# Optimization experiments

Hardware: AMD Instinct MI355X
Metric: run time of the kernel (lower is better)

The kernel has to match this reference:

```python
import jax, jax.numpy as jnp
import numpy as np

B, T, C, H = 8, 2048, 768, 64  # batch, block_size, n_embd, head_size

def setup_inputs() -> dict:
    key = jax.random.key(0)
    kx, kk, kq, kv = jax.random.split(key, 4)
    x = jax.random.normal(kx, (B, T, C), dtype=jnp.float32)
    Wk = jax.random.normal(kk, (C, H), dtype=jnp.float32) * (C ** -0.5)
    Wq = jax.random.normal(kq, (C, H), dtype=jnp.float32) * (C ** -0.5)
    Wv = jax.random.normal(kv, (C, H), dtype=jnp.float32) * (C ** -0.5)
    return {"x": x, "Wk": Wk, "Wq": Wq, "Wv": Wv}

def reference(x, Wk, Wq, Wv):
    # single causal self-attention head (dropout in eval mode = identity)
    k = jnp.einsum('btc,ch->bth', x, Wk)  # [B,T,H]
    q = jnp.einsum('btc,ch->bth', x, Wq)
    v = jnp.einsum('btc,ch->bth', x, Wv)
    scale = jnp.asarray(k.shape[-1], x.dtype) ** -0.5
    wei = jnp.einsum('bth,bsh->bts', q, k) * scale  # [B,T,T]
    t = x.shape[1]
    causal = jnp.tril(jnp.ones((t, t), dtype=bool))
    wei = jnp.where(causal[None, :, :], wei, jnp.asarray(-jnp.inf, wei.dtype))
    wei = jax.nn.softmax(wei, axis=-1)
    out = jnp.einsum('bts,bsh->bth', wei, v)  # [B,T,H]
    return out
```

## Files before the change

### kernel.cpp

```cpp
#include <hip/hip_runtime.h>
#include <hip/hip_bf16.h>

typedef __attribute__((ext_vector_type(8))) short short8;
typedef __attribute__((ext_vector_type(4))) float f32x4;

#define B_  8
#define T_  2048
#define C_  768
#define H_  64
#define M_  (B_ * T_)

static __device__ __forceinline__ unsigned short f2bf(float f) {
    __hip_bfloat16 h = __float2bfloat16(f);
    return *reinterpret_cast<unsigned short*>(&h);
}

static __device__ __forceinline__ short8 make_frag(const unsigned short* p0, const unsigned short* p1) {
    const ushort4 a = *reinterpret_cast<const ushort4*>(p0);
    const ushort4 b = *reinterpret_cast<const ushort4*>(p1);
    short8 r;
    r[0] = (short)a.x; r[1] = (short)a.y; r[2] = (short)a.z; r[3] = (short)a.w;
    r[4] = (short)b.x; r[5] = (short)b.y; r[6] = (short)b.z; r[7] = (short)b.w;
    return r;
}

static __device__ __forceinline__ int swz(int row, int u) {
    return row * 64 + ((((u) >> 3) ^ (row & 7)) << 3) + (u & 7);
}

__global__ __launch_bounds__(256) void prep_w(
    const float* __restrict__ Wq, const float* __restrict__ Wk, const float* __restrict__ Wv,
    unsigned short* __restrict__ Wt) {

    const int t   = threadIdx.x;
    const int mat = blockIdx.x / 48;
    const int kb  = blockIdx.x % 48;
    const int h   = t & 63;
    const int k0  = (kb * 4 + (t >> 6)) * 4;

    const float* Ws = (mat == 0) ? Wq : (mat == 1) ? Wk : Wv;
    ushort4 o;
    o.x = f2bf(Ws[(size_t)(k0 + 0) * H_ + h]);
    o.y = f2bf(Ws[(size_t)(k0 + 1) * H_ + h]);
    o.z = f2bf(Ws[(size_t)(k0 + 2) * H_ + h]);
    o.w = f2bf(Ws[(size_t)(k0 + 3) * H_ + h]);
    *reinterpret_cast<ushort4*>(&Wt[(size_t)(mat * 64 + h) * C_ + k0]) = o;
}

__global__ __launch_bounds__(256) void proj_kernel(
    const float* __restrict__ x, const unsigned short* __restrict__ Wt,
    unsigned short* __restrict__ qkv) {

    __shared__ unsigned short Als[4 * 12 * 512];

    const int tid = threadIdx.x;
    const int w   = tid >> 6;
    const int l   = tid & 63;
    const int lg  = l >> 4;
    const int lc  = l & 15;
    const int row0 = blockIdx.x * 64;

    const int sr  = tid >> 2;
    const int so  = tid & 3;
    const int srt = sr >> 4;
    const int sr15 = sr & 15;
    const int sbase = (so * 16 + (sr15 ^ so)) * 8;

    f32x4 acc[4][3];
#pragma unroll
    for (int rt = 0; rt < 4; ++rt)
#pragma unroll
        for (int ct = 0; ct < 3; ++ct) acc[rt][ct] = (f32x4)0.f;

    const unsigned short* bbase[3];
#pragma unroll
    for (int ct = 0; ct < 3; ++ct)
        bbase[ct] = Wt + (size_t)(w * 48 + ct * 16 + lc) * C_ + lg * 8;

    for (int phase = 0; phase < 2; ++phase) {
        if (phase) __syncthreads();
#pragma unroll
        for (int g = 0; g < 3; ++g) {
            float4 fa[4][2];
#pragma unroll
            for (int jj = 0; jj < 4; ++jj) {
                const int j = g * 4 + jj;
                const float* xp = x + (size_t)(row0 + sr) * C_ + phase * 384 + j * 32 + so * 8;
                fa[jj][0] = *reinterpret_cast<const float4*>(xp);
                fa[jj][1] = *reinterpret_cast<const float4*>(xp + 4);
            }
#pragma unroll
            for (int jj = 0; jj < 4; ++jj) {
                const int j = g * 4 + jj;
                short8 v;
                v[0] = (short)f2bf(fa[jj][0].x); v[1] = (short)f2bf(fa[jj][0].y);
                v[2] = (short)f2bf(fa[jj][0].z); v[3] = (short)f2bf(fa[jj][0].w);
                v[4] = (short)f2bf(fa[jj][1].x); v[5] = (short)f2bf(fa[jj][1].y);
                v[6] = (short)f2bf(fa[jj][1].z); v[7] = (short)f2bf(fa[jj][1].w);
                *reinterpret_cast<short8*>(&Als[(srt * 12 + j) * 512 + sbase]) = v;
            }
        }
        __syncthreads();

        short8 bcur[3], bnxt[3];
#pragma unroll
        for (int ct = 0; ct < 3; ++ct)
            bcur[ct] = *reinterpret_cast<const short8*>(bbase[ct] + phase * 384);

#pragma unroll
        for (int kk = 0; kk < 12; ++kk) {
            if (kk < 11) {
#pragma unroll
                for (int ct = 0; ct < 3; ++ct)
                    bnxt[ct] = *reinterpret_cast<const short8*>(bbase[ct] + phase * 384 + (kk + 1) * 32);
            }
            short8 af[4];
#pragma unroll
            for (int rt = 0; rt < 4; ++rt)
                af[rt] = *reinterpret_cast<const short8*>(
                    &Als[(rt * 12 + kk) * 512 + (lg * 16 + (lc ^ lg)) * 8]);
#pragma unroll
            for (int rt = 0; rt < 4; ++rt)
#pragma unroll
                for (int ct = 0; ct < 3; ++ct)
                    acc[rt][ct] = __builtin_amdgcn_mfma_f32_16x16x32_bf16(af[rt], bcur[ct], acc[rt][ct], 0, 0, 0);
            if (kk < 11) {
#pragma unroll
                for (int ct = 0; ct < 3; ++ct) bcur[ct] = bnxt[ct];
            }
        }
    }

#pragma unroll
    for (int ct = 0; ct < 3; ++ct) {
        const int col = w * 48 + ct * 16 + lc;
        const int mat = col >> 6;
        const int h   = col & 63;
#pragma unroll
        for (int rt = 0; rt < 4; ++rt)
#pragma unroll
            for (int j = 0; j < 4; ++j) {
                const int grow = row0 + rt * 16 + lg * 4 + j;
                qkv[(size_t)mat * (M_ * H_) + (size_t)grow * H_ + h] = f2bf(acc[rt][ct][j]);
            }
    }
}

#define SEG_FLOATS 4224
#define LOG2E_SCALE 0.18033688011112042f

template<int SEG>
static __device__ __forceinline__ int segs_per_batch() { return SEG == 32 ? 32 : 80; }

template<int SEG>
static __device__ __forceinline__ void decode_seg(int r, int& qt, int& seg) {
    if (SEG == 32) { qt = r; seg = 0; return; }
    if (r < 8)       { qt = r;                seg = 0; }
    else if (r < 24) { qt = 8  + (r - 8) / 2; seg = (r - 8) & 1; }
    else if (r < 48) { qt = 16 + (r - 24) / 3; seg = (r - 24) % 3; }
    else             { qt = 24 + (r - 48) / 4; seg = (r - 48) & 3; }
}

template<int SEG>
static __device__ __forceinline__ int seg_prefix(int qt) {
    if (SEG == 32) return qt;
    if (qt < 8)  return qt;
    if (qt < 16) return 8  + 2 * (qt - 8);
    if (qt < 24) return 24 + 3 * (qt - 16);
    return 48 + 4 * (qt - 24);
}

template<int SEG>
__global__ __launch_bounds__(256) void attn_partial(
    const unsigned short* __restrict__ qkv, float* __restrict__ part) {

    const int spb = segs_per_batch<SEG>();
    const int b   = blockIdx.x / spb;
    const int r_  = blockIdx.x % spb;
    int qt, seg;
    decode_seg<SEG>(r_, qt, seg);

    const int tid = threadIdx.x;
    const int w  = tid >> 6;
    const int l  = tid & 63;
    const int lg = l >> 4;
    const int lc = l & 15;

    __shared__ unsigned short Kl[64 * 64];
    __shared__ unsigned short Vt[64 * 64];

    const unsigned short* Qg = qkv;
    const unsigned short* Kg = qkv + (size_t)M_ * H_;
    const unsigned short* Vg = qkv + (size_t)2 * M_ * H_;

    const unsigned short* qrow = Qg + (size_t)(b * T_ + qt * 64 + w * 16 + lc) * H_;
    short8 qf[2];
#pragma unroll
    for (int ks = 0; ks < 2; ++ks)
        qf[ks] = make_frag(qrow + ks * 32 + lg * 4, qrow + ks * 32 + lg * 4 + 16);

    float mval = -1e30f, lsum = 0.f;
    f32x4 oT[4];
#pragma unroll
    for (int t = 0; t < 4; ++t) oT[t] = (f32x4)0.f;

    const int q_glob = qt * 64 + w * 16 + lc;

    const int kv_beg = seg * SEG;
    const int kv_end = min(kv_beg + SEG, qt + 1);

    for (int kv = kv_beg; kv < kv_end; ++kv) {
        __syncthreads();
#pragma unroll
        for (int rep = 0; rep < 2; ++rep) {
            const int idx = rep * 256 + tid;
            const int s   = idx >> 3;
            const int c16 = idx & 7;
            const size_t g = (size_t)(b * T_ + kv * 64 + s) * H_ + c16 * 8;
            short8 kvec = *reinterpret_cast<const short8*>(&Kg[g]);
            *reinterpret_cast<short8*>(&Kl[s * 64 + ((c16 ^ (s & 7)) << 3)]) = kvec;
        }
#pragma unroll
        for (int rep = 0; rep < 2; ++rep) {
            const int idx = rep * 256 + tid;
            const int s2  = idx >> 4;
            const int h0  = (idx & 15) * 4;
            const int s   = 2 * s2;
            const size_t g = (size_t)(b * T_ + kv * 64 + s) * H_ + h0;
            ushort4 v0 = *reinterpret_cast<const ushort4*>(&Vg[g]);
            ushort4 v1 = *reinterpret_cast<const ushort4*>(&Vg[g + H_]);
#pragma unroll
            for (int j = 0; j < 4; ++j) {
                const int h = h0 + j;
                unsigned int pk = (unsigned int)(&v0.x)[j] | ((unsigned int)(&v1.x)[j] << 16);
                *reinterpret_cast<unsigned int*>(&Vt[swz(h, s)]) = pk;
            }
        }
        __syncthreads();

        f32x4 sT[4];
#pragma unroll
        for (int st = 0; st < 4; ++st) {
            f32x4 accs = (f32x4)0.f;
#pragma unroll
            for (int ks = 0; ks < 2; ++ks) {
                const short8 kf = make_frag(&Kl[swz(st * 16 + lc, ks * 32 + lg * 4)],
                                            &Kl[swz(st * 16 + lc, ks * 32 + lg * 4 + 16)]);
                accs = __builtin_amdgcn_mfma_f32_16x16x32_bf16(kf, qf[ks], accs, 0, 0, 0);
            }
            sT[st] = accs;
        }

        float p[4][4];
#pragma unroll
        for (int st = 0; st < 4; ++st)
#pragma unroll
            for (int r = 0; r < 4; ++r)
                p[st][r] = sT[st][r] * LOG2E_SCALE;

        if (kv == qt) {
#pragma unroll
            for (int st = 0; st < 4; ++st)
#pragma unroll
                for (int r = 0; r < 4; ++r)
                    if ((kv * 64 + st * 16 + lg * 4 + r) > q_glob) p[st][r] = -1e30f;
        }

        float pm[4];
#pragma unroll
        for (int st = 0; st < 4; ++st)
            pm[st] = fmaxf(fmaxf(p[st][0], p[st][1]), fmaxf(p[st][2], p[st][3]));
        float pmax = fmaxf(fmaxf(pm[0], pm[1]), fmaxf(pm[2], pm[3]));
        pmax = fmaxf(pmax, __shfl_xor(pmax, 16));
        pmax = fmaxf(pmax, __shfl_xor(pmax, 32));

        const float mnew  = fmaxf(mval, pmax);
        const float alpha = exp2f(mval - mnew);
        mval = mnew;

        float ps[4];
#pragma unroll
        for (int st = 0; st < 4; ++st) {
#pragma unroll
            for (int r = 0; r < 4; ++r)
                p[st][r] = exp2f(p[st][r] - mnew);
            ps[st] = (p[st][0] + p[st][1]) + (p[st][2] + p[st][3]);
        }
        float srow = (ps[0] + ps[1]) + (ps[2] + ps[3]);
        srow += __shfl_xor(srow, 16);
        srow += __shfl_xor(srow, 32);
        lsum = lsum * alpha + srow;

#pragma unroll
        for (int ht = 0; ht < 4; ++ht) oT[ht] *= alpha;

        short8 pb[2];
#pragma unroll
        for (int ks = 0; ks < 2; ++ks) {
#pragma unroll
            for (int r = 0; r < 4; ++r) {
                pb[ks][r]     = (short)f2bf(p[2 * ks][r]);
                pb[ks][r + 4] = (short)f2bf(p[2 * ks + 1][r]);
            }
        }

#pragma unroll
        for (int ks = 0; ks < 2; ++ks) {
#pragma unroll
            for (int ht = 0; ht < 4; ++ht) {
                const short8 vf = make_frag(&Vt[swz(ht * 16 + lc, ks * 32 + lg * 4)],
                                            &Vt[swz(ht * 16 + lc, ks * 32 + lg * 4 + 16)]);
                oT[ht] = __builtin_amdgcn_mfma_f32_16x16x32_bf16(vf, pb[ks], oT[ht], 0, 0, 0);
            }
        }
    }

    float* base = part + (size_t)blockIdx.x * SEG_FLOATS;
#pragma unroll
    for (int ht = 0; ht < 4; ++ht)
        *reinterpret_cast<f32x4*>(&base[(w * 16 + lc) * 64 + ht * 16 + lg * 4]) = oT[ht];
    if (lg == 0) {
        base[4096 + w * 16 + lc] = mval;
        base[4160 + w * 16 + lc] = lsum;
    }
}

template<int SEG>
__global__ __launch_bounds__(256) void attn_merge(
    const float* __restrict__ part, float* __restrict__ out) {

    const int b  = blockIdx.x >> 5;
    const int qt = blockIdx.x & 31;
    const int nseg = (SEG == 32) ? 1 : (qt / 8 + 1);
    const int spb  = segs_per_batch<SEG>();
    const float* base0 = part + (size_t)(b * spb + seg_prefix<SEG>(qt)) * SEG_FLOATS;

    const int tid = threadIdx.x;
    const int row = tid >> 2;
    const int c0  = (tid & 3) * 16;

    float M = -1e30f;
    for (int s = 0; s < nseg; ++s)
        M = fmaxf(M, base0[(size_t)s * SEG_FLOATS + 4096 + row]);

    float L = 0.f;
    f32x4 acc[4];
#pragma unroll
    for (int k = 0; k < 4; ++k) acc[k] = (f32x4)0.f;

    for (int s = 0; s < nseg; ++s) {
        const float* sb = base0 + (size_t)s * SEG_FLOATS;
        const float wsc = exp2f(sb[4096 + row] - M);
        L += sb[4160 + row] * wsc;
#pragma unroll
        for (int k = 0; k < 4; ++k) {
            const f32x4 ov = *reinterpret_cast<const f32x4*>(&sb[row * 64 + c0 + 4 * k]);
            acc[k] += ov * wsc;
        }
    }
    const float inv = 1.f / L;
    float* op = out + (size_t)(b * T_ + qt * 64 + row) * H_ + c0;
#pragma unroll
    for (int k = 0; k < 4; ++k)
        *reinterpret_cast<f32x4*>(&op[4 * k]) = acc[k] * inv;
}

__global__ __launch_bounds__(256) void attn_kernel(
    const unsigned short* __restrict__ qkv, float* __restrict__ out) {

    const int b  = blockIdx.x >> 5;
    const int qt = blockIdx.x & 31;
    const int tid = threadIdx.x;
    const int w  = tid >> 6;
    const int l  = tid & 63;
    const int lg = l >> 4;
    const int lc = l & 15;

    __shared__ unsigned short Kl[64 * 64];
    __shared__ unsigned short Vt[64 * 64];

    const unsigned short* Qg = qkv;
    const unsigned short* Kg = qkv + (size_t)M_ * H_;
    const unsigned short* Vg = qkv + (size_t)2 * M_ * H_;

    const unsigned short* qrow = Qg + (size_t)(b * T_ + qt * 64 + w * 16 + lc) * H_;
    short8 qf[2];
#pragma unroll
    for (int ks = 0; ks < 2; ++ks)
        qf[ks] = make_frag(qrow + ks * 32 + lg * 4, qrow + ks * 32 + lg * 4 + 16);

    float mval = -1e30f, lsum = 0.f;
    f32x4 oT[4];
#pragma unroll
    for (int t = 0; t < 4; ++t) oT[t] = (f32x4)0.f;

    const int q_glob = qt * 64 + w * 16 + lc;

    for (int kv = 0; kv <= qt; ++kv) {
        __syncthreads();
#pragma unroll
        for (int rep = 0; rep < 2; ++rep) {
            const int idx = rep * 256 + tid;
            const int s   = idx >> 3;
            const int c16 = idx & 7;
            const size_t g = (size_t)(b * T_ + kv * 64 + s) * H_ + c16 * 8;
            short8 kvec = *reinterpret_cast<const short8*>(&Kg[g]);
            *reinterpret_cast<short8*>(&Kl[s * 64 + ((c16 ^ (s & 7)) << 3)]) = kvec;
        }
#pragma unroll
        for (int rep = 0; rep < 2; ++rep) {
            const int idx = rep * 256 + tid;
            const int s2  = idx >> 4;
            const int h0  = (idx & 15) * 4;
            const int s   = 2 * s2;
            const size_t g = (size_t)(b * T_ + kv * 64 + s) * H_ + h0;
            ushort4 v0 = *reinterpret_cast<const ushort4*>(&Vg[g]);
            ushort4 v1 = *reinterpret_cast<const ushort4*>(&Vg[g + H_]);
#pragma unroll
            for (int j = 0; j < 4; ++j) {
                const int h = h0 + j;
                unsigned int pk = (unsigned int)(&v0.x)[j] | ((unsigned int)(&v1.x)[j] << 16);
                *reinterpret_cast<unsigned int*>(&Vt[swz(h, s)]) = pk;
            }
        }
        __syncthreads();

        f32x4 sT[4];
#pragma unroll
        for (int st = 0; st < 4; ++st) {
            f32x4 accs = (f32x4)0.f;
#pragma unroll
            for (int ks = 0; ks < 2; ++ks) {
                const short8 kf = make_frag(&Kl[swz(st * 16 + lc, ks * 32 + lg * 4)],
                                            &Kl[swz(st * 16 + lc, ks * 32 + lg * 4 + 16)]);
                accs = __builtin_amdgcn_mfma_f32_16x16x32_bf16(kf, qf[ks], accs, 0, 0, 0);
            }
            sT[st] = accs;
        }

        float p[4][4];
#pragma unroll
        for (int st = 0; st < 4; ++st)
#pragma unroll
            for (int r = 0; r < 4; ++r)
                p[st][r] = sT[st][r] * LOG2E_SCALE;

        if (kv == qt) {
#pragma unroll
            for (int st = 0; st < 4; ++st)
#pragma unroll
                for (int r = 0; r < 4; ++r)
                    if ((kv * 64 + st * 16 + lg * 4 + r) > q_glob) p[st][r] = -1e30f;
        }

        float pm[4];
#pragma unroll
        for (int st = 0; st < 4; ++st)
            pm[st] = fmaxf(fmaxf(p[st][0], p[st][1]), fmaxf(p[st][2], p[st][3]));
        float pmax = fmaxf(fmaxf(pm[0], pm[1]), fmaxf(pm[2], pm[3]));
        pmax = fmaxf(pmax, __shfl_xor(pmax, 16));
        pmax = fmaxf(pmax, __shfl_xor(pmax, 32));

        const float mnew  = fmaxf(mval, pmax);
        const float alpha = exp2f(mval - mnew);
        mval = mnew;

        float ps[4];
#pragma unroll
        for (int st = 0; st < 4; ++st) {
#pragma unroll
            for (int r = 0; r < 4; ++r)
                p[st][r] = exp2f(p[st][r] - mnew);
            ps[st] = (p[st][0] + p[st][1]) + (p[st][2] + p[st][3]);
        }
        float srow = (ps[0] + ps[1]) + (ps[2] + ps[3]);
        srow += __shfl_xor(srow, 16);
        srow += __shfl_xor(srow, 32);
        lsum = lsum * alpha + srow;

#pragma unroll
        for (int ht = 0; ht < 4; ++ht) oT[ht] *= alpha;

        short8 pb[2];
#pragma unroll
        for (int ks = 0; ks < 2; ++ks) {
#pragma unroll
            for (int r = 0; r < 4; ++r) {
                pb[ks][r]     = (short)f2bf(p[2 * ks][r]);
                pb[ks][r + 4] = (short)f2bf(p[2 * ks + 1][r]);
            }
        }

#pragma unroll
        for (int ks = 0; ks < 2; ++ks) {
#pragma unroll
            for (int ht = 0; ht < 4; ++ht) {
                const short8 vf = make_frag(&Vt[swz(ht * 16 + lc, ks * 32 + lg * 4)],
                                            &Vt[swz(ht * 16 + lc, ks * 32 + lg * 4 + 16)]);
                oT[ht] = __builtin_amdgcn_mfma_f32_16x16x32_bf16(vf, pb[ks], oT[ht], 0, 0, 0);
            }
        }
    }

    const float inv = 1.f / lsum;
    float* op = out + (size_t)(b * T_ + q_glob) * H_;
#pragma unroll
    for (int ht = 0; ht < 4; ++ht) {
        f32x4 v = oT[ht] * inv;
        *reinterpret_cast<f32x4*>(&op[ht * 16 + lg * 4]) = v;
    }
}

extern "C" void kernel_launch(void* const* d_in, const int* in_sizes, int n_in,
                              void* d_out, int out_size, void* d_ws, size_t ws_size,
                              hipStream_t stream) {
    const float* x  = (const float*)d_in[0];
    const float* Wk = (const float*)d_in[1];
    const float* Wq = (const float*)d_in[2];
    const float* Wv = (const float*)d_in[3];

    const size_t qkvB = (size_t)3 * M_ * H_ * 2;
    const size_t WtB  = (size_t)3 * H_ * C_ * 2;
    unsigned short* qkv = (unsigned short*)d_ws;
    unsigned short* Wt  = (unsigned short*)((char*)d_ws + qkvB);
    float* part = (float*)((char*)d_ws + qkvB + WtB);
    float* out  = (float*)d_out;

    prep_w<<<dim3(144), dim3(256), 0, stream>>>(Wq, Wk, Wv, Wt);
    proj_kernel<<<dim3(M_ / 64), dim3(256), 0, stream>>>(x, Wt, qkv);

    const size_t need8  = qkvB + WtB + (size_t)(B_ * 80) * SEG_FLOATS * 4;
    const size_t need32 = qkvB + WtB + (size_t)(B_ * 32) * SEG_FLOATS * 4;
    if (ws_size >= need8) {
        attn_partial<8><<<dim3(B_ * 80), dim3(256), 0, stream>>>(qkv, part);
        attn_merge<8><<<dim3(B_ * 32), dim3(256), 0, stream>>>(part, out);
    } else if (ws_size >= need32) {
        attn_partial<32><<<dim3(B_ * 32), dim3(256), 0, stream>>>(qkv, part);
        attn_merge<32><<<dim3(B_ * 32), dim3(256), 0, stream>>>(part, out);
    } else {
        attn_kernel<<<dim3(B_ * 32), dim3(256), 0, stream>>>(qkv, out);
    }
}
```

Baseline: 64.34 us.

## Halve projection row tile, prefetch K/V tiles into registers, skip redundant rescale

The projection kernel now handles 32 rows per block instead of 64, which doubles the grid and halves LDS use and accumulator registers, so more blocks can be resident. The attention partial kernel loads the next K/V tile into registers while computing on the current tile in shared memory, overlapping global loads with MFMA and softmax work. Both attention kernels skip the online-softmax rescale when no row maximum grew, avoiding the exp2 and the multiplies over the output accumulators. The costs are extra registers for the prefetch buffers and a wave-wide vote per iteration.

```diff
diff --git a/kernel.cpp b/kernel.cpp
--- a/kernel.cpp
+++ b/kernel.cpp
@@ -51,24 +51,23 @@
     const float* __restrict__ x, const unsigned short* __restrict__ Wt,
     unsigned short* __restrict__ qkv) {
 
-    __shared__ unsigned short Als[4 * 12 * 512];
+    __shared__ unsigned short Als[2 * 12 * 512];
 
     const int tid = threadIdx.x;
     const int w   = tid >> 6;
     const int l   = tid & 63;
     const int lg  = l >> 4;
     const int lc  = l & 15;
-    const int row0 = blockIdx.x * 64;
-
-    const int sr  = tid >> 2;
-    const int so  = tid & 3;
-    const int srt = sr >> 4;
+    const int row0 = blockIdx.x * 32;
+
+    const int sr   = tid >> 3;
+    const int so   = tid & 7;
+    const int srt  = sr >> 4;
     const int sr15 = sr & 15;
-    const int sbase = (so * 16 + (sr15 ^ so)) * 8;
-
-    f32x4 acc[4][3];
-#pragma unroll
-    for (int rt = 0; rt < 4; ++rt)
+
+    f32x4 acc[2][3];
+#pragma unroll
+    for (int rt = 0; rt < 2; ++rt)
 #pragma unroll
         for (int ct = 0; ct < 3; ++ct) acc[rt][ct] = (f32x4)0.f;
 
@@ -79,26 +78,25 @@
 
     for (int phase = 0; phase < 2; ++phase) {
         if (phase) __syncthreads();
-#pragma unroll
-        for (int g = 0; g < 3; ++g) {
-            float4 fa[4][2];
-#pragma unroll
-            for (int jj = 0; jj < 4; ++jj) {
-                const int j = g * 4 + jj;
-                const float* xp = x + (size_t)(row0 + sr) * C_ + phase * 384 + j * 32 + so * 8;
-                fa[jj][0] = *reinterpret_cast<const float4*>(xp);
-                fa[jj][1] = *reinterpret_cast<const float4*>(xp + 4);
-            }
-#pragma unroll
-            for (int jj = 0; jj < 4; ++jj) {
-                const int j = g * 4 + jj;
-                short8 v;
-                v[0] = (short)f2bf(fa[jj][0].x); v[1] = (short)f2bf(fa[jj][0].y);
-                v[2] = (short)f2bf(fa[jj][0].z); v[3] = (short)f2bf(fa[jj][0].w);
-                v[4] = (short)f2bf(fa[jj][1].x); v[5] = (short)f2bf(fa[jj][1].y);
-                v[6] = (short)f2bf(fa[jj][1].z); v[7] = (short)f2bf(fa[jj][1].w);
-                *reinterpret_cast<short8*>(&Als[(srt * 12 + j) * 512 + sbase]) = v;
-            }
+        float4 fa[6][2];
+#pragma unroll
+        for (int g = 0; g < 6; ++g) {
+            const float* xp = x + (size_t)(row0 + sr) * C_ + phase * 384 + (so + 8 * g) * 8;
+            fa[g][0] = *reinterpret_cast<const float4*>(xp);
+            fa[g][1] = *reinterpret_cast<const float4*>(xp + 4);
+        }
+#pragma unroll
+        for (int g = 0; g < 6; ++g) {
+            const int j8  = so + 8 * g;
+            const int kk  = j8 >> 2;
+            const int so4 = j8 & 3;
+            short8 v;
+            v[0] = (short)f2bf(fa[g][0].x); v[1] = (short)f2bf(fa[g][0].y);
+            v[2] = (short)f2bf(fa[g][0].z); v[3] = (short)f2bf(fa[g][0].w);
+            v[4] = (short)f2bf(fa[g][1].x); v[5] = (short)f2bf(fa[g][1].y);
+            v[6] = (short)f2bf(fa[g][1].z); v[7] = (short)f2bf(fa[g][1].w);
+            *reinterpret_cast<short8*>(
+                &Als[(srt * 12 + kk) * 512 + (so4 * 16 + (sr15 ^ so4)) * 8]) = v;
         }
         __syncthreads();
 
@@ -114,13 +112,13 @@
                 for (int ct = 0; ct < 3; ++ct)
                     bnxt[ct] = *reinterpret_cast<const short8*>(bbase[ct] + phase * 384 + (kk + 1) * 32);
             }
-            short8 af[4];
-#pragma unroll
-            for (int rt = 0; rt < 4; ++rt)
+            short8 af[2];
+#pragma unroll
+            for (int rt = 0; rt < 2; ++rt)
                 af[rt] = *reinterpret_cast<const short8*>(
                     &Als[(rt * 12 + kk) * 512 + (lg * 16 + (lc ^ lg)) * 8]);
 #pragma unroll
-            for (int rt = 0; rt < 4; ++rt)
+            for (int rt = 0; rt < 2; ++rt)
 #pragma unroll
                 for (int ct = 0; ct < 3; ++ct)
                     acc[rt][ct] = __builtin_amdgcn_mfma_f32_16x16x32_bf16(af[rt], bcur[ct], acc[rt][ct], 0, 0, 0);
@@ -137,7 +135,7 @@
         const int mat = col >> 6;
         const int h   = col & 63;
 #pragma unroll
-        for (int rt = 0; rt < 4; ++rt)
+        for (int rt = 0; rt < 2; ++rt)
 #pragma unroll
             for (int j = 0; j < 4; ++j) {
                 const int grow = row0 + rt * 16 + lg * 4 + j;
@@ -193,6 +191,16 @@
     const unsigned short* Kg = qkv + (size_t)M_ * H_;
     const unsigned short* Vg = qkv + (size_t)2 * M_ * H_;
 
+    const int sK0 = tid >> 3;
+    const int c16 = tid & 7;
+    const int kOff  = sK0 * H_ + c16 * 8;
+    const int kLds0 = sK0 * 64 + ((c16 ^ (sK0 & 7)) << 3);
+    const int kLds1 = (sK0 + 32) * 64 + ((c16 ^ ((sK0 + 32) & 7)) << 3);
+
+    const int sV0 = 2 * (tid >> 4);
+    const int h0  = (tid & 15) * 4;
+    const int vOff = sV0 * H_ + h0;
+
     const unsigned short* qrow = Qg + (size_t)(b * T_ + qt * 64 + w * 16 + lc) * H_;
     short8 qf[2];
 #pragma unroll
@@ -209,7 +217,197 @@
     const int kv_beg = seg * SEG;
     const int kv_end = min(kv_beg + SEG, qt + 1);
 
+    short8  kreg0, kreg1;
+    ushort4 va0, vb0, va1, vb1;
+
+    auto load_tiles = [&](int kv) {
+        const size_t off = (size_t)(b * T_ + kv * 64) * H_;
+        kreg0 = *reinterpret_cast<const short8*>(&Kg[off + kOff]);
+        kreg1 = *reinterpret_cast<const short8*>(&Kg[off + kOff + 32 * H_]);
+        va0 = *reinterpret_cast<const ushort4*>(&Vg[off + vOff]);
+        vb0 = *reinterpret_cast<const ushort4*>(&Vg[off + vOff + H_]);
+        va1 = *reinterpret_cast<const ushort4*>(&Vg[off + vOff + 32 * H_]);
+        vb1 = *reinterpret_cast<const ushort4*>(&Vg[off + vOff + 32 * H_ + H_]);
+    };
+
+    load_tiles(kv_beg);
+
     for (int kv = kv_beg; kv < kv_end; ++kv) {
+        __syncthreads();
+        *reinterpret_cast<short8*>(&Kl[kLds0]) = kreg0;
+        *reinterpret_cast<short8*>(&Kl[kLds1]) = kreg1;
+#pragma unroll
+        for (int j = 0; j < 4; ++j) {
+            const unsigned int p0 = (unsigned int)(&va0.x)[j] | ((unsigned int)(&vb0.x)[j] << 16);
+            *reinterpret_cast<unsigned int*>(&Vt[swz(h0 + j, sV0)]) = p0;
+            const unsigned int p1 = (unsigned int)(&va1.x)[j] | ((unsigned int)(&vb1.x)[j] << 16);
+            *reinterpret_cast<unsigned int*>(&Vt[swz(h0 + j, sV0 + 32)]) = p1;
+        }
+        __syncthreads();
+
+        if (kv + 1 < kv_end) load_tiles(kv + 1);
+
+        f32x4 sT[4];
+#pragma unroll
+        for (int st = 0; st < 4; ++st) {
+            f32x4 accs = (f32x4)0.f;
+#pragma unroll
+            for (int ks = 0; ks < 2; ++ks) {
+                const short8 kf = make_frag(&Kl[swz(st * 16 + lc, ks * 32 + lg * 4)],
+                                            &Kl[swz(st * 16 + lc, ks * 32 + lg * 4 + 16)]);
+                accs = __builtin_amdgcn_mfma_f32_16x16x32_bf16(kf, qf[ks], accs, 0, 0, 0);
+            }
+            sT[st] = accs;
+        }
+
+        float p[4][4];
+#pragma unroll
+        for (int st = 0; st < 4; ++st)
+#pragma unroll
+            for (int r = 0; r < 4; ++r)
+                p[st][r] = sT[st][r] * LOG2E_SCALE;
+
+        if (kv == qt) {
+#pragma unroll
+            for (int st = 0; st < 4; ++st)
+#pragma unroll
+                for (int r = 0; r < 4; ++r)
+                    if ((kv * 64 + st * 16 + lg * 4 + r) > q_glob) p[st][r] = -1e30f;
+        }
+
+        float pm[4];
+#pragma unroll
+        for (int st = 0; st < 4; ++st)
+            pm[st] = fmaxf(fmaxf(p[st][0], p[st][1]), fmaxf(p[st][2], p[st][3]));
+        float pmax = fmaxf(fmaxf(pm[0], pm[1]), fmaxf(pm[2], pm[3]));
+        pmax = fmaxf(pmax, __shfl_xor(pmax, 16));
+        pmax = fmaxf(pmax, __shfl_xor(pmax, 32));
+
+        if (!__all(pmax <= mval)) {
+            const float mnew  = fmaxf(mval, pmax);
+            const float alpha = exp2f(mval - mnew);
+            mval = mnew;
+            lsum *= alpha;
+#pragma unroll
+            for (int ht = 0; ht < 4; ++ht) oT[ht] *= alpha;
+        }
+
+        float ps[4];
+#pragma unroll
+        for (int st = 0; st < 4; ++st) {
+#pragma unroll
+            for (int r = 0; r < 4; ++r)
+                p[st][r] = exp2f(p[st][r] - mval);
+            ps[st] = (p[st][0] + p[st][1]) + (p[st][2] + p[st][3]);
+        }
+        float srow = (ps[0] + ps[1]) + (ps[2] + ps[3]);
+        srow += __shfl_xor(srow, 16);
+        srow += __shfl_xor(srow, 32);
+        lsum += srow;
+
+        short8 pb[2];
+#pragma unroll
+        for (int ks = 0; ks < 2; ++ks) {
+#pragma unroll
+            for (int r = 0; r < 4; ++r) {
+                pb[ks][r]     = (short)f2bf(p[2 * ks][r]);
+                pb[ks][r + 4] = (short)f2bf(p[2 * ks + 1][r]);
+            }
+        }
+
+#pragma unroll
+        for (int ks = 0; ks < 2; ++ks) {
+#pragma unroll
+            for (int ht = 0; ht < 4; ++ht) {
+                const short8 vf = make_frag(&Vt[swz(ht * 16 + lc, ks * 32 + lg * 4)],
+                                            &Vt[swz(ht * 16 + lc, ks * 32 + lg * 4 + 16)]);
+                oT[ht] = __builtin_amdgcn_mfma_f32_16x16x32_bf16(vf, pb[ks], oT[ht], 0, 0, 0);
+            }
+        }
+    }
+
+    float* base = part + (size_t)blockIdx.x * SEG_FLOATS;
+#pragma unroll
+    for (int ht = 0; ht < 4; ++ht)
+        *reinterpret_cast<f32x4*>(&base[(w * 16 + lc) * 64 + ht * 16 + lg * 4]) = oT[ht];
+    if (lg == 0) {
+        base[4096 + w * 16 + lc] = mval;
+        base[4160 + w * 16 + lc] = lsum;
+    }
+}
+
+template<int SEG>
+__global__ __launch_bounds__(256) void attn_merge(
+    const float* __restrict__ part, float* __restrict__ out) {
+
+    const int b  = blockIdx.x >> 5;
+    const int qt = blockIdx.x & 31;
+    const int nseg = (SEG == 32) ? 1 : (qt / 8 + 1);
+    const int spb  = segs_per_batch<SEG>();
+    const float* base0 = part + (size_t)(b * spb + seg_prefix<SEG>(qt)) * SEG_FLOATS;
+
+    const int tid = threadIdx.x;
+    const int row = tid >> 2;
+    const int c0  = (tid & 3) * 16;
+
+    float M = -1e30f;
+    for (int s = 0; s < nseg; ++s)
+        M = fmaxf(M, base0[(size_t)s * SEG_FLOATS + 4096 + row]);
+
+    float L = 0.f;
+    f32x4 acc[4];
+#pragma unroll
+    for (int k = 0; k < 4; ++k) acc[k] = (f32x4)0.f;
+
+    for (int s = 0; s < nseg; ++s) {
+        const float* sb = base0 + (size_t)s * SEG_FLOATS;
+        const float wsc = exp2f(sb[4096 + row] - M);
+        L += sb[4160 + row] * wsc;
+#pragma unroll
+        for (int k = 0; k < 4; ++k) {
+            const f32x4 ov = *reinterpret_cast<const f32x4*>(&sb[row * 64 + c0 + 4 * k]);
+            acc[k] += ov * wsc;
+        }
+    }
+    const float inv = 1.f / L;
+    float* op = out + (size_t)(b * T_ + qt * 64 + row) * H_ + c0;
+#pragma unroll
+    for (int k = 0; k < 4; ++k)
+        *reinterpret_cast<f32x4*>(&op[4 * k]) = acc[k] * inv;
+}
+
+__global__ __launch_bounds__(256) void attn_kernel(
+    const unsigned short* __restrict__ qkv, float* __restrict__ out) {
+
+    const int b  = blockIdx.x >> 5;
+    const int qt = blockIdx.x & 31;
+    const int tid = threadIdx.x;
+    const int w  = tid >> 6;
+    const int l  = tid & 63;
+    const int lg = l >> 4;
+    const int lc = l & 15;
+
+    __shared__ unsigned short Kl[64 * 64];
+    __shared__ unsigned short Vt[64 * 64];
+
+    const unsigned short* Qg = qkv;
+    const unsigned short* Kg = qkv + (size_t)M_ * H_;
+    const unsigned short* Vg = qkv + (size_t)2 * M_ * H_;
+
+    const unsigned short* qrow = Qg + (size_t)(b * T_ + qt * 64 + w * 16 + lc) * H_;
+    short8 qf[2];
+#pragma unroll
+    for (int ks = 0; ks < 2; ++ks)
+        qf[ks] = make_frag(qrow + ks * 32 + lg * 4, qrow + ks * 32 + lg * 4 + 16);
+
+    float mval = -1e30f, lsum = 0.f;
+    f32x4 oT[4];
+#pragma unroll
+    for (int t = 0; t < 4; ++t) oT[t] = (f32x4)0.f;
+
+    const int q_glob = qt * 64 + w * 16 + lc;
+
+    for (int kv = 0; kv <= qt; ++kv) {
         __syncthreads();
 #pragma unroll
         for (int rep = 0; rep < 2; ++rep) {
@@ -274,212 +472,27 @@
         pmax = fmaxf(pmax, __shfl_xor(pmax, 16));
         pmax = fmaxf(pmax, __shfl_xor(pmax, 32));
 
-        const float mnew  = fmaxf(mval, pmax);
-        const float alpha = exp2f(mval - mnew);
-        mval = mnew;
+        if (!__all(pmax <= mval)) {
+            const float mnew  = fmaxf(mval, pmax);
+            const float alpha = exp2f(mval - mnew);
+            mval = mnew;
+            lsum *= alpha;
+#pragma unroll
+            for (int ht = 0; ht < 4; ++ht) oT[ht] *= alpha;
+        }
 
         float ps[4];
 #pragma unroll
         for (int st = 0; st < 4; ++st) {
 #pragma unroll
             for (int r = 0; r < 4; ++r)
-                p[st][r] = exp2f(p[st][r] - mnew);
+                p[st][r] = exp2f(p[st][r] - mval);
             ps[st] = (p[st][0] + p[st][1]) + (p[st][2] + p[st][3]);
         }
         float srow = (ps[0] + ps[1]) + (ps[2] + ps[3]);
         srow += __shfl_xor(srow, 16);
         srow += __shfl_xor(srow, 32);
-        lsum = lsum * alpha + srow;
-
-#pragma unroll
-        for (int ht = 0; ht < 4; ++ht) oT[ht] *= alpha;
-
-        short8 pb[2];
-#pragma unroll
-        for (int ks = 0; ks < 2; ++ks) {
-#pragma unroll
-            for (int r = 0; r < 4; ++r) {
-                pb[ks][r]     = (short)f2bf(p[2 * ks][r]);
-                pb[ks][r + 4] = (short)f2bf(p[2 * ks + 1][r]);
-            }
-        }
-
-#pragma unroll
-        for (int ks = 0; ks < 2; ++ks) {
-#pragma unroll
-            for (int ht = 0; ht < 4; ++ht) {
-                const short8 vf = make_frag(&Vt[swz(ht * 16 + lc, ks * 32 + lg * 4)],
-                                            &Vt[swz(ht * 16 + lc, ks * 32 + lg * 4 + 16)]);
-                oT[ht] = __builtin_amdgcn_mfma_f32_16x16x32_bf16(vf, pb[ks], oT[ht], 0, 0, 0);
-            }
-        }
-    }
-
-    float* base = part + (size_t)blockIdx.x * SEG_FLOATS;
-#pragma unroll
-    for (int ht = 0; ht < 4; ++ht)
-        *reinterpret_cast<f32x4*>(&base[(w * 16 + lc) * 64 + ht * 16 + lg * 4]) = oT[ht];
-    if (lg == 0) {
-        base[4096 + w * 16 + lc] = mval;
-        base[4160 + w * 16 + lc] = lsum;
-    }
-}
-
-template<int SEG>
-__global__ __launch_bounds__(256) void attn_merge(
-    const float* __restrict__ part, float* __restrict__ out) {
-
-    const int b  = blockIdx.x >> 5;
-    const int qt = blockIdx.x & 31;
-    const int nseg = (SEG == 32) ? 1 : (qt / 8 + 1);
-    const int spb  = segs_per_batch<SEG>();
-    const float* base0 = part + (size_t)(b * spb + seg_prefix<SEG>(qt)) * SEG_FLOATS;
-
-    const int tid = threadIdx.x;
-    const int row = tid >> 2;
-    const int c0  = (tid & 3) * 16;
-
-    float M = -1e30f;
-    for (int s = 0; s < nseg; ++s)
-        M = fmaxf(M, base0[(size_t)s * SEG_FLOATS + 4096 + row]);
-
-    float L = 0.f;
-    f32x4 acc[4];
-#pragma unroll
-    for (int k = 0; k < 4; ++k) acc[k] = (f32x4)0.f;
-
-    for (int s = 0; s < nseg; ++s) {
-        const float* sb = base0 + (size_t)s * SEG_FLOATS;
-        const float wsc = exp2f(sb[4096 + row] - M);
-        L += sb[4160 + row] * wsc;
-#pragma unroll
-        for (int k = 0; k < 4; ++k) {
-            const f32x4 ov = *reinterpret_cast<const f32x4*>(&sb[row * 64 + c0 + 4 * k]);
-            acc[k] += ov * wsc;
-        }
-    }
-    const float inv = 1.f / L;
-    float* op = out + (size_t)(b * T_ + qt * 64 + row) * H_ + c0;
-#pragma unroll
-    for (int k = 0; k < 4; ++k)
-        *reinterpret_cast<f32x4*>(&op[4 * k]) = acc[k] * inv;
-}
-
-__global__ __launch_bounds__(256) void attn_kernel(
-    const unsigned short* __restrict__ qkv, float* __restrict__ out) {
-
-    const int b  = blockIdx.x >> 5;
-    const int qt = blockIdx.x & 31;
-    const int tid = threadIdx.x;
-    const int w  = tid >> 6;
-    const int l  = tid & 63;
-    const int lg = l >> 4;
-    const int lc = l & 15;
-
-    __shared__ unsigned short Kl[64 * 64];
-    __shared__ unsigned short Vt[64 * 64];
-
-    const unsigned short* Qg = qkv;
-    const unsigned short* Kg = qkv + (size_t)M_ * H_;
-    const unsigned short* Vg = qkv + (size_t)2 * M_ * H_;
-
-    const unsigned short* qrow = Qg + (size_t)(b * T_ + qt * 64 + w * 16 + lc) * H_;
-    short8 qf[2];
-#pragma unroll
-    for (int ks = 0; ks < 2; ++ks)
-        qf[ks] = make_frag(qrow + ks * 32 + lg * 4, qrow + ks * 32 + lg * 4 + 16);
-
-    float mval = -1e30f, lsum = 0.f;
-    f32x4 oT[4];
-#pragma unroll
-    for (int t = 0; t < 4; ++t) oT[t] = (f32x4)0.f;
-
-    const int q_glob = qt * 64 + w * 16 + lc;
-
-    for (int kv = 0; kv <= qt; ++kv) {
-        __syncthreads();
-#pragma unroll
-        for (int rep = 0; rep < 2; ++rep) {
-            const int idx = rep * 256 + tid;
-            const int s   = idx >> 3;
-            const int c16 = idx & 7;
-            const size_t g = (size_t)(b * T_ + kv * 64 + s) * H_ + c16 * 8;
-            short8 kvec = *reinterpret_cast<const short8*>(&Kg[g]);
-            *reinterpret_cast<short8*>(&Kl[s * 64 + ((c16 ^ (s & 7)) << 3)]) = kvec;
-        }
-#pragma unroll
-        for (int rep = 0; rep < 2; ++rep) {
-            const int idx = rep * 256 + tid;
-            const int s2  = idx >> 4;
-            const int h0  = (idx & 15) * 4;
-            const int s   = 2 * s2;
-            const size_t g = (size_t)(b * T_ + kv * 64 + s) * H_ + h0;
-            ushort4 v0 = *reinterpret_cast<const ushort4*>(&Vg[g]);
-            ushort4 v1 = *reinterpret_cast<const ushort4*>(&Vg[g + H_]);
-#pragma unroll
-            for (int j = 0; j < 4; ++j) {
-                const int h = h0 + j;
-                unsigned int pk = (unsigned int)(&v0.x)[j] | ((unsigned int)(&v1.x)[j] << 16);
-                *reinterpret_cast<unsigned int*>(&Vt[swz(h, s)]) = pk;
-            }
-        }
-        __syncthreads();
-
-        f32x4 sT[4];
-#pragma unroll
-        for (int st = 0; st < 4; ++st) {
-            f32x4 accs = (f32x4)0.f;
-#pragma unroll
-            for (int ks = 0; ks < 2; ++ks) {
-                const short8 kf = make_frag(&Kl[swz(st * 16 + lc, ks * 32 + lg * 4)],
-                                            &Kl[swz(st * 16 + lc, ks * 32 + lg * 4 + 16)]);
-                accs = __builtin_amdgcn_mfma_f32_16x16x32_bf16(kf, qf[ks], accs, 0, 0, 0);
-            }
-            sT[st] = accs;
-        }
-
-        float p[4][4];
-#pragma unroll
-        for (int st = 0; st < 4; ++st)
-#pragma unroll
-            for (int r = 0; r < 4; ++r)
-                p[st][r] = sT[st][r] * LOG2E_SCALE;
-
-        if (kv == qt) {
-#pragma unroll
-            for (int st = 0; st < 4; ++st)
-#pragma unroll
-                for (int r = 0; r < 4; ++r)
-                    if ((kv * 64 + st * 16 + lg * 4 + r) > q_glob) p[st][r] = -1e30f;
-        }
-
-        float pm[4];
-#pragma unroll
-        for (int st = 0; st < 4; ++st)
-            pm[st] = fmaxf(fmaxf(p[st][0], p[st][1]), fmaxf(p[st][2], p[st][3]));
-        float pmax = fmaxf(fmaxf(pm[0], pm[1]), fmaxf(pm[2], pm[3]));
-        pmax = fmaxf(pmax, __shfl_xor(pmax, 16));
-        pmax = fmaxf(pmax, __shfl_xor(pmax, 32));
-
-        const float mnew  = fmaxf(mval, pmax);
-        const float alpha = exp2f(mval - mnew);
-        mval = mnew;
-
-        float ps[4];
-#pragma unroll
-        for (int st = 0; st < 4; ++st) {
-#pragma unroll
-            for (int r = 0; r < 4; ++r)
-                p[st][r] = exp2f(p[st][r] - mnew);
-            ps[st] = (p[st][0] + p[st][1]) + (p[st][2] + p[st][3]);
-        }
-        float srow = (ps[0] + ps[1]) + (ps[2] + ps[3]);
-        srow += __shfl_xor(srow, 16);
-        srow += __shfl_xor(srow, 32);
-        lsum = lsum * alpha + srow;
-
-#pragma unroll
-        for (int ht = 0; ht < 4; ++ht) oT[ht] *= alpha;
+        lsum += srow;
 
         short8 pb[2];
 #pragma unroll
@@ -527,7 +540,7 @@
     float* out  = (float*)d_out;
 
     prep_w<<<dim3(144), dim3(256), 0, stream>>>(Wq, Wk, Wv, Wt);
-    proj_kernel<<<dim3(M_ / 64), dim3(256), 0, stream>>>(x, Wt, qkv);
+    proj_kernel<<<dim3(M_ / 32), dim3(256), 0, stream>>>(x, Wt, qkv);
 
     const size_t need8  = qkvB + WtB + (size_t)(B_ * 80) * SEG_FLOATS * 4;
     const size_t need32 = qkvB + WtB + (size_t)(B_ * 32) * SEG_FLOATS * 4;
```

After: 66.84 us. 3.9% more time.

## Pre-swizzle K/V tiles in projection and double-buffer attention loads via global_load_lds

Applied to the files above, without the earlier changes.

The projection kernel now writes K and V in per-64-row tile images that already carry the swizzled LDS layout, with V stored transposed. The attention kernels can then copy tiles straight into shared memory. The partial-attention kernel double-buffers K/V with direct global-to-LDS loads, prefetching the next tile while computing the current one, and manual waitcnt and barriers replace the transpose-and-store staging. Both attention kernels also skip the online-softmax rescale when no row max grows. This adds scattered, uncoalesced stores in the projection epilogue and depends on hand-written vmcnt accounting being correct.

```diff
diff --git a/kernel.cpp b/kernel.cpp
--- a/kernel.cpp
+++ b/kernel.cpp
@@ -9,6 +9,10 @@
 #define C_  768
 #define H_  64
 #define M_  (B_ * T_)
+
+#define GLDS16(g, l) __builtin_amdgcn_global_load_lds(                        \
+    (const __attribute__((address_space(1))) void*)(g),                       \
+    (__attribute__((address_space(3))) void*)(l), 16, 0, 0)
 
 static __device__ __forceinline__ unsigned short f2bf(float f) {
     __hip_bfloat16 h = __float2bfloat16(f);
@@ -60,9 +64,9 @@
     const int lc  = l & 15;
     const int row0 = blockIdx.x * 64;
 
-    const int sr  = tid >> 2;
-    const int so  = tid & 3;
-    const int srt = sr >> 4;
+    const int sr   = tid >> 2;
+    const int so   = tid & 3;
+    const int srt  = sr >> 4;
     const int sr15 = sr & 15;
     const int sbase = (so * 16 + (sr15 ^ so)) * 8;
 
@@ -131,6 +135,9 @@
         }
     }
 
+    unsigned short* Qd   = qkv;
+    unsigned short* Kimg = qkv + (size_t)M_ * H_;
+    unsigned short* Vimg = qkv + (size_t)2 * M_ * H_;
 #pragma unroll
     for (int ct = 0; ct < 3; ++ct) {
         const int col = w * 48 + ct * 16 + lc;
@@ -141,7 +148,15 @@
 #pragma unroll
             for (int j = 0; j < 4; ++j) {
                 const int grow = row0 + rt * 16 + lg * 4 + j;
-                qkv[(size_t)mat * (M_ * H_) + (size_t)grow * H_ + h] = f2bf(acc[rt][ct][j]);
+                const unsigned short v = f2bf(acc[rt][ct][j]);
+                if (mat == 0) {
+                    Qd[(size_t)grow * H_ + h] = v;
+                } else {
+                    const int g  = grow >> 6;
+                    const int s6 = grow & 63;
+                    if (mat == 1) Kimg[((size_t)g << 12) + swz(s6, h)] = v;
+                    else          Vimg[((size_t)g << 12) + swz(h, s6)] = v;
+                }
             }
     }
 }
@@ -186,8 +201,8 @@
     const int lg = l >> 4;
     const int lc = l & 15;
 
-    __shared__ unsigned short Kl[64 * 64];
-    __shared__ unsigned short Vt[64 * 64];
+    __shared__ unsigned short Kls[2][4096];
+    __shared__ unsigned short Vls[2][4096];
 
     const unsigned short* Qg = qkv;
     const unsigned short* Kg = qkv + (size_t)M_ * H_;
@@ -209,34 +224,36 @@
     const int kv_beg = seg * SEG;
     const int kv_end = min(kv_beg + SEG, qt + 1);
 
+    const int go = w * 1024 + l * 8;
+
+    auto stage = [&](int buf, int kv) {
+        const size_t tb = ((size_t)(b * 32 + kv)) << 12;
+        const unsigned short* kt = Kg + tb;
+        const unsigned short* vt = Vg + tb;
+        GLDS16(kt + go,       &Kls[buf][w * 1024]);
+        GLDS16(kt + go + 512, &Kls[buf][w * 1024 + 512]);
+        GLDS16(vt + go,       &Vls[buf][w * 1024]);
+        GLDS16(vt + go + 512, &Vls[buf][w * 1024 + 512]);
+    };
+
+    stage(0, kv_beg);
+    int cur = 0;
+
     for (int kv = kv_beg; kv < kv_end; ++kv) {
-        __syncthreads();
-#pragma unroll
-        for (int rep = 0; rep < 2; ++rep) {
-            const int idx = rep * 256 + tid;
-            const int s   = idx >> 3;
-            const int c16 = idx & 7;
-            const size_t g = (size_t)(b * T_ + kv * 64 + s) * H_ + c16 * 8;
-            short8 kvec = *reinterpret_cast<const short8*>(&Kg[g]);
-            *reinterpret_cast<short8*>(&Kl[s * 64 + ((c16 ^ (s & 7)) << 3)]) = kvec;
-        }
-#pragma unroll
-        for (int rep = 0; rep < 2; ++rep) {
-            const int idx = rep * 256 + tid;
-            const int s2  = idx >> 4;
-            const int h0  = (idx & 15) * 4;
-            const int s   = 2 * s2;
-            const size_t g = (size_t)(b * T_ + kv * 64 + s) * H_ + h0;
-            ushort4 v0 = *reinterpret_cast<const ushort4*>(&Vg[g]);
-            ushort4 v1 = *reinterpret_cast<const ushort4*>(&Vg[g + H_]);
-#pragma unroll
-            for (int j = 0; j < 4; ++j) {
-                const int h = h0 + j;
-                unsigned int pk = (unsigned int)(&v0.x)[j] | ((unsigned int)(&v1.x)[j] << 16);
-                *reinterpret_cast<unsigned int*>(&Vt[swz(h, s)]) = pk;
-            }
-        }
-        __syncthreads();
+        const bool more = (kv + 1 < kv_end);
+        __builtin_amdgcn_s_barrier();
+        asm volatile("" ::: "memory");
+        if (more) {
+            stage(cur ^ 1, kv + 1);
+            asm volatile("s_waitcnt vmcnt(4)" ::: "memory");
+        } else {
+            asm volatile("s_waitcnt vmcnt(0)" ::: "memory");
+        }
+        __builtin_amdgcn_s_barrier();
+        asm volatile("" ::: "memory");
+
+        const unsigned short* Kc = Kls[cur];
+        const unsigned short* Vc = Vls[cur];
 
         f32x4 sT[4];
 #pragma unroll
@@ -244,8 +261,8 @@
             f32x4 accs = (f32x4)0.f;
 #pragma unroll
             for (int ks = 0; ks < 2; ++ks) {
-                const short8 kf = make_frag(&Kl[swz(st * 16 + lc, ks * 32 + lg * 4)],
-                                            &Kl[swz(st * 16 + lc, ks * 32 + lg * 4 + 16)]);
+                const short8 kf = make_frag(&Kc[swz(st * 16 + lc, ks * 32 + lg * 4)],
+                                            &Kc[swz(st * 16 + lc, ks * 32 + lg * 4 + 16)]);
                 accs = __builtin_amdgcn_mfma_f32_16x16x32_bf16(kf, qf[ks], accs, 0, 0, 0);
             }
             sT[st] = accs;
@@ -274,25 +291,27 @@
         pmax = fmaxf(pmax, __shfl_xor(pmax, 16));
         pmax = fmaxf(pmax, __shfl_xor(pmax, 32));
 
-        const float mnew  = fmaxf(mval, pmax);
-        const float alpha = exp2f(mval - mnew);
-        mval = mnew;
+        if (!__all(pmax <= mval)) {
+            const float mnew  = fmaxf(mval, pmax);
+            const float alpha = exp2f(mval - mnew);
+            mval = mnew;
+            lsum *= alpha;
+#pragma unroll
+            for (int ht = 0; ht < 4; ++ht) oT[ht] *= alpha;
+        }
 
         float ps[4];
 #pragma unroll
         for (int st = 0; st < 4; ++st) {
 #pragma unroll
             for (int r = 0; r < 4; ++r)
-                p[st][r] = exp2f(p[st][r] - mnew);
+                p[st][r] = exp2f(p[st][r] - mval);
             ps[st] = (p[st][0] + p[st][1]) + (p[st][2] + p[st][3]);
         }
         float srow = (ps[0] + ps[1]) + (ps[2] + ps[3]);
         srow += __shfl_xor(srow, 16);
         srow += __shfl_xor(srow, 32);
-        lsum = lsum * alpha + srow;
-
-#pragma unroll
-        for (int ht = 0; ht < 4; ++ht) oT[ht] *= alpha;
+        lsum += srow;
 
         short8 pb[2];
 #pragma unroll
@@ -308,11 +327,12 @@
         for (int ks = 0; ks < 2; ++ks) {
 #pragma unroll
             for (int ht = 0; ht < 4; ++ht) {
-                const short8 vf = make_frag(&Vt[swz(ht * 16 + lc, ks * 32 + lg * 4)],
-                                            &Vt[swz(ht * 16 + lc, ks * 32 + lg * 4 + 16)]);
+                const short8 vf = make_frag(&Vc[swz(ht * 16 + lc, ks * 32 + lg * 4)],
+                                            &Vc[swz(ht * 16 + lc, ks * 32 + lg * 4 + 16)]);
                 oT[ht] = __builtin_amdgcn_mfma_f32_16x16x32_bf16(vf, pb[ks], oT[ht], 0, 0, 0);
             }
         }
+        cur ^= 1;
     }
 
     float* base = part + (size_t)blockIdx.x * SEG_FLOATS;
@@ -376,8 +396,8 @@
     const int lg = l >> 4;
     const int lc = l & 15;
 
-    __shared__ unsigned short Kl[64 * 64];
-    __shared__ unsigned short Vt[64 * 64];
+    __shared__ unsigned short Kl[4096];
+    __shared__ unsigned short Vt[4096];
 
     const unsigned short* Qg = qkv;
     const unsigned short* Kg = qkv + (size_t)M_ * H_;
@@ -398,31 +418,11 @@
 
     for (int kv = 0; kv <= qt; ++kv) {
         __syncthreads();
-#pragma unroll
-        for (int rep = 0; rep < 2; ++rep) {
-            const int idx = rep * 256 + tid;
-            const int s   = idx >> 3;
-            const int c16 = idx & 7;
-            const size_t g = (size_t)(b * T_ + kv * 64 + s) * H_ + c16 * 8;
-            short8 kvec = *reinterpret_cast<const short8*>(&Kg[g]);
-            *reinterpret_cast<short8*>(&Kl[s * 64 + ((c16 ^ (s & 7)) << 3)]) = kvec;
-        }
-#pragma unroll
-        for (int rep = 0; rep < 2; ++rep) {
-            const int idx = rep * 256 + tid;
-            const int s2  = idx >> 4;
-            const int h0  = (idx & 15) * 4;
-            const int s   = 2 * s2;
-            const size_t g = (size_t)(b * T_ + kv * 64 + s) * H_ + h0;
-            ushort4 v0 = *reinterpret_cast<const ushort4*>(&Vg[g]);
-            ushort4 v1 = *reinterpret_cast<const ushort4*>(&Vg[g + H_]);
-#pragma unroll
-            for (int j = 0; j < 4; ++j) {
-                const int h = h0 + j;
-                unsigned int pk = (unsigned int)(&v0.x)[j] | ((unsigned int)(&v1.x)[j] << 16);
-                *reinterpret_cast<unsigned int*>(&Vt[swz(h, s)]) = pk;
-            }
-        }
+        const size_t tb = ((size_t)(b * 32 + kv)) << 12;
+        reinterpret_cast<short8*>(Kl)[tid]       = reinterpret_cast<const short8*>(Kg + tb)[tid];
+        reinterpret_cast<short8*>(Kl)[tid + 256] = reinterpret_cast<const short8*>(Kg + tb)[tid + 256];
+        reinterpret_cast<short8*>(Vt)[tid]       = reinterpret_cast<const short8*>(Vg + tb)[tid];
+        reinterpret_cast<short8*>(Vt)[tid + 256] = reinterpret_cast<const short8*>(Vg + tb)[tid + 256];
         __syncthreads();
 
         f32x4 sT[4];
@@ -461,25 +461,27 @@
         pmax = fmaxf(pmax, __shfl_xor(pmax, 16));
         pmax = fmaxf(pmax, __shfl_xor(pmax, 32));
 
-        const float mnew  = fmaxf(mval, pmax);
-        const float alpha = exp2f(mval - mnew);
-        mval = mnew;
+        if (!__all(pmax <= mval)) {
+            const float mnew  = fmaxf(mval, pmax);
+            const float alpha = exp2f(mval - mnew);
+            mval = mnew;
+            lsum *= alpha;
+#pragma unroll
+            for (int ht = 0; ht < 4; ++ht) oT[ht] *= alpha;
+        }
 
         float ps[4];
 #pragma unroll
         for (int st = 0; st < 4; ++st) {
 #pragma unroll
             for (int r = 0; r < 4; ++r)
-                p[st][r] = exp2f(p[st][r] - mnew);
+                p[st][r] = exp2f(p[st][r] - mval);
             ps[st] = (p[st][0] + p[st][1]) + (p[st][2] + p[st][3]);
         }
         float srow = (ps[0] + ps[1]) + (ps[2] + ps[3]);
         srow += __shfl_xor(srow, 16);
         srow += __shfl_xor(srow, 32);
-        lsum = lsum * alpha + srow;
-
-#pragma unroll
-        for (int ht = 0; ht < 4; ++ht) oT[ht] *= alpha;
+        lsum += srow;
 
         short8 pb[2];
 #pragma unroll
```

New measurement: 58.38 us. 9.3% less time.
